# Optimization experiments

Measured on AMD Instinct MI355X. Metric: run time of the kernel, lower is better.

Reference implementation:

```python
import jax, jax.numpy as jnp
import numpy as np

N = 50000      # nodes
E = 800000     # edges
F = 64         # in_channels == out_channels
ED = 16        # edge_dim
G = 64         # graphs in batch
L = 2          # numLayers
BN_EPS = 1e-5
STD_EPS = 1e-5
AGG_DIM = F * 4 * 3  # 4 aggregators x 3 scalers


def setup_inputs() -> dict:
    key = jax.random.key(0)
    ks = jax.random.split(key, 12)
    r = lambda k, shp, fan: (jax.random.normal(k, shp, jnp.float32) / np.sqrt(fan)).astype(jnp.float32)
    return dict(
        x=jax.random.normal(ks[0], (N, F), jnp.float32),
        edge_attr=jax.random.normal(ks[1], (E, ED), jnp.float32),
        We=r(ks[2], (L, ED, F), ED), be=jnp.zeros((L, F), jnp.float32),
        Wpre=r(ks[3], (L, 3 * F, F), 3 * F), bpre=jnp.zeros((L, F), jnp.float32),
        Wpost=r(ks[4], (L, F + AGG_DIM, F), F + AGG_DIM), bpost=jnp.zeros((L, F), jnp.float32),
        Wlin=r(ks[5], (L, F, F), F), blin=jnp.zeros((L, F), jnp.float32),
        gamma=jnp.ones((L, F), jnp.float32), beta=jnp.zeros((L, F), jnp.float32),
        W1=r(ks[6], (F, 40), F), b1=jnp.zeros((40,), jnp.float32),
        W2=r(ks[7], (40, 1), 40), b2=jnp.zeros((1,), jnp.float32),
        edge_index=jax.random.randint(ks[8], (2, E), 0, N),
        batch=jnp.sort(jax.random.randint(ks[9], (N,), 0, G)),
    )


def _ceal_conv(x, src, dst, edge_attr, We, be, Wpre, bpre, Wpost, bpost, Wlin, blin, deg, amp, att):
    # PNA-style conv, towers=1, pre_layers=post_layers=1
    e = edge_attr @ We + be                                              # [E,F]
    h = jnp.concatenate([x[dst], x[src], e], axis=-1) @ Wpre + bpre      # [E,F]
    degc = jnp.maximum(deg, 1.0)[:, None]
    mean = jax.ops.segment_sum(h, dst, num_segments=N) / degc
    sq = jax.ops.segment_sum(h * h, dst, num_segments=N) / degc
    std = jnp.sqrt(jax.nn.relu(sq - mean * mean) + STD_EPS)
    has = (deg > 0)[:, None]
    mn = jnp.where(has, jax.ops.segment_min(h, dst, num_segments=N), 0.0)
    mx = jnp.where(has, jax.ops.segment_max(h, dst, num_segments=N), 0.0)
    aggs = jnp.concatenate([mean, mn, mx, std], axis=-1)                 # [N,4F]
    scaled = jnp.concatenate([aggs, aggs * amp[:, None], aggs * att[:, None]], axis=-1)  # [N,12F]
    out = jnp.concatenate([x, scaled], axis=-1) @ Wpost + bpost          # [N,F]
    return out @ Wlin + blin


def _bn(x, gamma, beta):
    mu = x.mean(0)
    var = x.var(0)  # biased, as torch BatchNorm training-mode normalization
    return (x - mu) * jax.lax.rsqrt(var + BN_EPS) * gamma + beta


def reference(x, edge_attr, We, be, Wpre, bpre, Wpost, bpost, Wlin, blin,
              gamma, beta, W1, b1, W2, b2, edge_index, batch):
    src, dst = edge_index[0], edge_index[1]
    deg = jax.ops.segment_sum(jnp.ones((E,), jnp.float32), dst, num_segments=N)
    avg_log = jnp.mean(jnp.log(deg + 1.0))
    logd = jnp.log(jnp.maximum(deg, 1.0) + 1.0)
    amp = logd / avg_log
    att = avg_log / logd
    for l in range(L):
        x = _ceal_conv(x, src, dst, edge_attr, We[l], be[l], Wpre[l], bpre[l],
                       Wpost[l], bpost[l], Wlin[l], blin[l], deg, amp, att)
        x = jax.nn.relu(_bn(x, gamma[l], beta[l]))
    cnt = jnp.maximum(jax.ops.segment_sum(jnp.ones((N,), jnp.float32), batch, num_segments=G), 1.0)
    gm = jax.ops.segment_sum(x, batch, num_segments=G) / cnt[:, None]    # global_mean_pool [G,F]
    return jax.nn.relu(gm @ W1 + b1) @ W2 + b2                           # [G,1]
```

## Files before the change

### kernel.cpp

```cpp
#include <hip/hip_runtime.h>
#include <math.h>
#include <float.h>

#define NN 50000
#define EE 800000
#define FF 64
#define EDIM 16
#define GG 64
#define NB64 782
#define NSB 196

typedef short bf16x8 __attribute__((ext_vector_type(8)));
typedef float f32x4 __attribute__((ext_vector_type(4)));

__device__ inline unsigned short bf_rne(float v) {
  unsigned int u = __float_as_uint(v);
  unsigned int r = (u + 0x7FFFu + ((u >> 16) & 1u)) >> 16;
  return (unsigned short)r;
}
__device__ inline float bf_up(unsigned short h) {
  return __uint_as_float(((unsigned int)h) << 16);
}
__device__ inline void split4(float4 v, ushort4& h, ushort4& l) {
  h.x = bf_rne(v.x); h.y = bf_rne(v.y); h.z = bf_rne(v.z); h.w = bf_rne(v.w);
  l.x = bf_rne(v.x - bf_up(h.x));
  l.y = bf_rne(v.y - bf_up(h.y));
  l.z = bf_rne(v.z - bf_up(h.z));
  l.w = bf_rne(v.w - bf_up(h.w));
}
__device__ inline float blo(unsigned int u) { return __uint_as_float(u << 16); }
__device__ inline float bhi(unsigned int u) { return __uint_as_float(u & 0xFFFF0000u); }

__global__ void k_deg(const int* __restrict__ eidx, int* __restrict__ deg) {
  int e = blockIdx.x * 256 + threadIdx.x;
  if (e < EE) atomicAdd(&deg[eidx[EE + e]], 1);
}

__global__ __launch_bounds__(256) void k_scanA(const int* __restrict__ deg, int* __restrict__ offsets,
                                               int* __restrict__ bsum, float* __restrict__ lsum) {
  __shared__ int ws[4];
  __shared__ float lw[4];
  int t = threadIdx.x;
  int lane = t & 63;
  int wv = t >> 6;
  int i = blockIdx.x * 256 + t;
  int v = (i < NN) ? deg[i] : 0;
  float lg = (i < NN) ? logf((float)v + 1.0f) : 0.0f;
  int x = v;
  #pragma unroll
  for (int o = 1; o < 64; o <<= 1) {
    int y = __shfl_up(x, o);
    if (lane >= o) x += y;
  }
  #pragma unroll
  for (int o = 1; o < 64; o <<= 1) lg += __shfl_xor(lg, o);
  if (lane == 63) ws[wv] = x;
  if (lane == 0) lw[wv] = lg;
  __syncthreads();
  int pre = 0;
  for (int k = 0; k < wv; k++) pre += ws[k];
  if (i < NN) offsets[i] = pre + x - v;
  if (t == 0) {
    bsum[blockIdx.x] = ws[0] + ws[1] + ws[2] + ws[3];
    lsum[blockIdx.x] = lw[0] + lw[1] + lw[2] + lw[3];
  }
}

__global__ __launch_bounds__(256) void k_scanB(const int* __restrict__ bsum, const float* __restrict__ lsum,
                                               int* __restrict__ bpref, float* __restrict__ meta,
                                               float* __restrict__ scbA) {
  __shared__ int ws[4];
  __shared__ float lw[4];
  int t = threadIdx.x;
  int lane = t & 63;
  int wv = t >> 6;
  int v = (t < NSB) ? bsum[t] : 0;
  float lg = (t < NSB) ? lsum[t] : 0.0f;
  int x = v;
  #pragma unroll
  for (int o = 1; o < 64; o <<= 1) {
    int y = __shfl_up(x, o);
    if (lane >= o) x += y;
  }
  #pragma unroll
  for (int o = 1; o < 64; o <<= 1) lg += __shfl_xor(lg, o);
  if (lane == 63) ws[wv] = x;
  if (lane == 0) lw[wv] = lg;
  __syncthreads();
  int pre = 0;
  for (int k = 0; k < wv; k++) pre += ws[k];
  if (t < NSB) bpref[t] = pre + x - v;
  if (t == 0) meta[0] = (lw[0] + lw[1] + lw[2] + lw[3]) / (float)NN;
  if (t < 64) { scbA[t] = 1.0f; scbA[64 + t] = 0.0f; }
  if (t == 0) scbA[128] = -FLT_MAX;
}

__global__ __launch_bounds__(256) void k_scanC(int* __restrict__ offsets, const int* __restrict__ bpref,
                                               const int* __restrict__ deg, const float* __restrict__ meta,
                                               float* __restrict__ amp, float* __restrict__ att) {
  int i = blockIdx.x * 256 + threadIdx.x;
  if (i < NN) {
    offsets[i] += bpref[blockIdx.x];
    float d = (float)deg[i];
    float avg = meta[0];
    float logd = logf(fmaxf(d, 1.0f) + 1.0f);
    amp[i] = logd / avg;
    att[i] = avg / logd;
  }
  if (i == 0) offsets[NN] = EE;
}

__global__ void k_scatter(const int* __restrict__ eidx, const int* __restrict__ offsets,
                          int* __restrict__ cursor, int* __restrict__ srcs,
                          const float* __restrict__ eattr, unsigned int* __restrict__ PermEA) {
  int e = blockIdx.x * 256 + threadIdx.x;
  if (e < EE) {
    int s = eidx[e];
    int d = eidx[EE + e];
    int pos = offsets[d] + atomicAdd(&cursor[d], 1);
    srcs[pos] = s;
    const float4* ep = (const float4*)(eattr + (size_t)e * EDIM);
    float4 q0 = ep[0], q1 = ep[1], q2 = ep[2], q3 = ep[3];
    uint4 pa, pb;
    pa.x = (unsigned)bf_rne(q0.x) | ((unsigned)bf_rne(q0.y) << 16);
    pa.y = (unsigned)bf_rne(q0.z) | ((unsigned)bf_rne(q0.w) << 16);
    pa.z = (unsigned)bf_rne(q1.x) | ((unsigned)bf_rne(q1.y) << 16);
    pa.w = (unsigned)bf_rne(q1.z) | ((unsigned)bf_rne(q1.w) << 16);
    pb.x = (unsigned)bf_rne(q2.x) | ((unsigned)bf_rne(q2.y) << 16);
    pb.y = (unsigned)bf_rne(q2.z) | ((unsigned)bf_rne(q2.w) << 16);
    pb.z = (unsigned)bf_rne(q3.x) | ((unsigned)bf_rne(q3.y) << 16);
    pb.w = (unsigned)bf_rne(q3.z) | ((unsigned)bf_rne(q3.w) << 16);
    ((uint4*)PermEA)[(size_t)pos * 2] = pa;
    ((uint4*)PermEA)[(size_t)pos * 2 + 1] = pb;
  }
}

__global__ __launch_bounds__(256) void k_prep2(const float* __restrict__ We, const float* __restrict__ be,
                                               const float* __restrict__ Wpre, const float* __restrict__ bpre,
                                               const float* __restrict__ Wpost, const float* __restrict__ bpost,
                                               const float* __restrict__ Wlin, const float* __restrict__ blin,
                                               float* __restrict__ Mw, float* __restrict__ bconst,
                                               unsigned short* __restrict__ WcT_h, unsigned short* __restrict__ WcT_l,
                                               unsigned short* __restrict__ WxT_h, unsigned short* __restrict__ WxT_l,
                                               float* __restrict__ bcomb) {
  int id = blockIdx.x * 256 + threadIdx.x;
  if (id < 53248) {
    int k = id >> 6, f = id & 63;
    float a = 0.0f;
    for (int j = 0; j < FF; j++) a += Wpost[(size_t)k * FF + j] * Wlin[j * FF + f];
    unsigned short h = bf_rne(a);
    WcT_h[f * 832 + k] = h;
    WcT_l[f * 832 + k] = bf_rne(a - bf_up(h));
  } else if (id < 61440) {
    int lid = id - 53248;
    int j = lid >> 6, k = lid & 63;
    float v = (j < 64) ? Wpre[k * FF + j] : Wpre[(64 + k) * FF + (j - 64)];
    unsigned short h = bf_rne(v);
    WxT_h[j * 64 + k] = h;
    WxT_l[j * 64 + k] = bf_rne(v - bf_up(h));
  } else if (id < 62464) {
    int lid = id - 61440;
    int k = lid >> 6, f = lid & 63;
    float a = 0.0f;
    for (int j = 0; j < FF; j++) a += We[k * FF + j] * Wpre[(128 + j) * FF + f];
    Mw[k * FF + f] = a;
  } else {
    int f = threadIdx.x;
    if (blockIdx.x == 244 && f < 64) {
      float b = bpre[f];
      for (int j = 0; j < FF; j++) b += be[j] * Wpre[(128 + j) * FF + f];
      bconst[f] = b;
      float c = blin[f];
      for (int j = 0; j < FF; j++) c += bpost[j] * Wlin[j * FF + f];
      bcomb[f] = c;
    }
  }
}

__global__ __launch_bounds__(256) void k_xform(const float* __restrict__ x, const float* __restrict__ scb,
                                               const unsigned short* __restrict__ WxT_h,
                                               const unsigned short* __restrict__ WxT_l,
                                               float* __restrict__ Xd, unsigned short* __restrict__ Xs) {
  __shared__ unsigned short Ah[64 * 72], Al[64 * 72];
  __shared__ unsigned short Bh[128 * 72], Bl[128 * 72];
  int t = threadIdx.x;
  int n0 = blockIdx.x * 64;
  {
    int j = t >> 1, half = t & 1;
    const ushort4* srch = (const ushort4*)(WxT_h + j * 64 + half * 32);
    const ushort4* srcl = (const ushort4*)(WxT_l + j * 64 + half * 32);
    #pragma unroll
    for (int i = 0; i < 8; i++) {
      *(ushort4*)&Bh[j * 72 + half * 32 + i * 4] = srch[i];
      *(ushort4*)&Bl[j * 72 + half * 32 + i * 4] = srcl[i];
    }
  }
  {
    int r = t >> 2, c0 = (t & 3) * 16;
    int n = n0 + r;
    bool rok = n < NN;
    const float4* src = (const float4*)(x + (size_t)n * FF + c0);
    float flr = scb[128];
    #pragma unroll
    for (int c4 = 0; c4 < 4; c4++) {
      float4 v = rok ? src[c4] : make_float4(0.f, 0.f, 0.f, 0.f);
      float4 sc = ((const float4*)scb)[(c0 >> 2) + c4];
      float4 of = ((const float4*)(scb + 64))[(c0 >> 2) + c4];
      v.x = fmaxf(v.x * sc.x + of.x, flr);
      v.y = fmaxf(v.y * sc.y + of.y, flr);
      v.z = fmaxf(v.z * sc.z + of.z, flr);
      v.w = fmaxf(v.w * sc.w + of.w, flr);
      ushort4 h4, l4;
      split4(v, h4, l4);
      *(ushort4*)&Ah[r * 72 + c0 + c4 * 4] = h4;
      *(ushort4*)&Al[r * 72 + c0 + c4 * 4] = l4;
    }
  }
  __syncthreads();
  int lane = t & 63;
  int l15 = lane & 15;
  int quad = lane >> 4;
  int w = __builtin_amdgcn_readfirstlane(t >> 6);
  int rbase = (w & 1) * 32;
  int cbase = (w >> 1) * 64;
  f32x4 acc[2][4];
  #pragma unroll
  for (int rt = 0; rt < 2; rt++)
    #pragma unroll
    for (int ct = 0; ct < 4; ct++) acc[rt][ct] = (f32x4){0.f, 0.f, 0.f, 0.f};

  #pragma unroll
  for (int ks = 0; ks < 2; ks++) {
    bf16x8 a_h[2], a_l[2];
    #pragma unroll
    for (int rt = 0; rt < 2; rt++) {
      int row = rbase + rt * 16 + l15;
      a_h[rt] = *(const bf16x8*)&Ah[row * 72 + ks * 32 + quad * 8];
      a_l[rt] = *(const bf16x8*)&Al[row * 72 + ks * 32 + quad * 8];
    }
    #pragma unroll
    for (int ct = 0; ct < 4; ct++) {
      int col = cbase + ct * 16 + l15;
      bf16x8 b_h = *(const bf16x8*)&Bh[col * 72 + ks * 32 + quad * 8];
      bf16x8 b_l = *(const bf16x8*)&Bl[col * 72 + ks * 32 + quad * 8];
      #pragma unroll
      for (int rt = 0; rt < 2; rt++) {
        acc[rt][ct] = __builtin_amdgcn_mfma_f32_16x16x32_bf16(a_h[rt], b_h, acc[rt][ct], 0, 0, 0);
        acc[rt][ct] = __builtin_amdgcn_mfma_f32_16x16x32_bf16(a_h[rt], b_l, acc[rt][ct], 0, 0, 0);
        acc[rt][ct] = __builtin_amdgcn_mfma_f32_16x16x32_bf16(a_l[rt], b_h, acc[rt][ct], 0, 0, 0);
      }
    }
  }
  #pragma unroll
  for (int rt = 0; rt < 2; rt++) {
    #pragma unroll
    for (int ct = 0; ct < 4; ct++) {
      int col = cbase + ct * 16 + l15;
      #pragma unroll
      for (int reg = 0; reg < 4; reg++) {
        int n = n0 + rbase + rt * 16 + quad * 4 + reg;
        if (n < NN) {
          float v = acc[rt][ct][reg];
          if (col < 64) Xd[(size_t)n * FF + col] = v;
          else          Xs[(size_t)n * FF + (col - 64)] = bf_rne(v);
        }
      }
    }
  }
}

__global__ __launch_bounds__(256) void k_agg(const int* __restrict__ srcs, const int* __restrict__ offsets,
                                             const unsigned int* __restrict__ PermEA,
                                             const float* __restrict__ Mw, const float* __restrict__ bconst,
                                             const float* __restrict__ Xd, const unsigned short* __restrict__ Xs,
                                             unsigned short* __restrict__ aggs) {
  int wid = __builtin_amdgcn_readfirstlane(threadIdx.x >> 6);
  int lane = threadIdx.x & 63;
  int n = blockIdx.x * 4 + wid;
  if (n >= NN) return;
  float mw[16];
  #pragma unroll
  for (int k = 0; k < 16; k++) mw[k] = Mw[k * FF + lane];
  float base_h = Xd[(size_t)n * FF + lane] + bconst[lane];
  int o0 = offsets[n], o1 = offsets[n + 1];
  float s = 0.f, sq = 0.f, mn = FLT_MAX, mx = -FLT_MAX;

  for (int base = o0; base < o1; base += 64) {
    int m = min(64, o1 - base);
    int sv = 0;
    if (base + lane < o1) sv = srcs[base + lane];
    for (int j = 0; j < m; j++) {
      int src = __shfl(sv, j);
      float xs = bf_up(Xs[(size_t)src * FF + lane]);
      const uint4* q = (const uint4*)PermEA + (size_t)(base + j) * 2;
      uint4 qa = q[0], qb = q[1];
      float et = blo(qa.x) * mw[0]  + bhi(qa.x) * mw[1]
               + blo(qa.y) * mw[2]  + bhi(qa.y) * mw[3]
               + blo(qa.z) * mw[4]  + bhi(qa.z) * mw[5]
               + blo(qa.w) * mw[6]  + bhi(qa.w) * mw[7]
               + blo(qb.x) * mw[8]  + bhi(qb.x) * mw[9]
               + blo(qb.y) * mw[10] + bhi(qb.y) * mw[11]
               + blo(qb.z) * mw[12] + bhi(qb.z) * mw[13]
               + blo(qb.w) * mw[14] + bhi(qb.w) * mw[15];
      float h = base_h + xs + et;
      s += h;
      sq += h * h;
      mn = fminf(mn, h);
      mx = fmaxf(mx, h);
    }
  }
  float d = (float)(o1 - o0);
  float dc = fmaxf(d, 1.0f);
  float mean = s / dc;
  float msq = sq / dc;
  float sd = sqrtf(fmaxf(msq - mean * mean, 0.0f) + 1e-5f);
  bool has = d > 0.0f;
  float vmn = has ? mn : 0.0f;
  float vmx = has ? mx : 0.0f;
  size_t b = (size_t)n * 256;
  aggs[b + lane] = bf_rne(mean);
  aggs[b + 64 + lane] = bf_rne(vmn);
  aggs[b + 128 + lane] = bf_rne(vmx);
  aggs[b + 192 + lane] = bf_rne(sd);
}

__global__ __launch_bounds__(256) void k_post(const float* __restrict__ x, const float* __restrict__ scb,
                                              const unsigned short* __restrict__ aggs,
                                              const float* __restrict__ amp, const float* __restrict__ att,
                                              const unsigned short* __restrict__ WcT_h,
                                              const unsigned short* __restrict__ WcT_l,
                                              const float* __restrict__ bcomb,
                                              float* __restrict__ y, float* __restrict__ partials) {
  __shared__ unsigned short Ah[64 * 72], Al[64 * 72];
  __shared__ unsigned short Bh[64 * 72], Bl[64 * 72];
  __shared__ float red_s[4][32], red_q[4][32];
  int t = threadIdx.x;
  int n0 = blockIdx.x * 64;
  int lane = t & 63;
  int l15 = lane & 15;
  int quad = lane >> 4;
  int w = __builtin_amdgcn_readfirstlane(t >> 6);
  int rbase = (w & 1) * 32;
  int cbase = (w >> 1) * 32;

  int ar = t >> 2;
  int ac0 = (t & 3) * 16;
  int an = n0 + ar;
  bool rok = an < NN;
  float sc_amp = rok ? amp[an] : 0.f;
  float sc_att = rok ? att[an] : 0.f;
  const float* xrow = x + (size_t)an * FF;
  const unsigned short* arow = aggs + (size_t)an * 256;
  float flr = scb[128];

  f32x4 acc[2][2];
  #pragma unroll
  for (int rt = 0; rt < 2; rt++)
    #pragma unroll
    for (int ct = 0; ct < 2; ct++) acc[rt][ct] = (f32x4){0.f, 0.f, 0.f, 0.f};

  for (int kc = 0; kc < 13; kc++) {
    if (kc == 0) {
      #pragma unroll
      for (int c4 = 0; c4 < 4; c4++) {
        float4 v = rok ? *(const float4*)(xrow + ac0 + c4 * 4) : make_float4(0.f, 0.f, 0.f, 0.f);
        float4 sc = ((const float4*)scb)[(ac0 >> 2) + c4];
        float4 of = ((const float4*)(scb + 64))[(ac0 >> 2) + c4];
        v.x = fmaxf(v.x * sc.x + of.x, flr);
        v.y = fmaxf(v.y * sc.y + of.y, flr);
        v.z = fmaxf(v.z * sc.z + of.z, flr);
        v.w = fmaxf(v.w * sc.w + of.w, flr);
        ushort4 h4, l4;
        split4(v, h4, l4);
        *(ushort4*)&Ah[ar * 72 + ac0 + c4 * 4] = h4;
        *(ushort4*)&Al[ar * 72 + ac0 + c4 * 4] = l4;
      }
    } else {
      int kcm = kc - 1;
      const unsigned short* srcb = arow + (kcm & 3) * 64;
      int sel = kcm >> 2;
      float scale = (sel == 0) ? 1.0f : (sel == 1 ? sc_amp : sc_att);
      #pragma unroll
      for (int c4 = 0; c4 < 4; c4++) {
        ushort4 u = rok ? *(const ushort4*)(srcb + ac0 + c4 * 4) : make_ushort4(0, 0, 0, 0);
        ushort4 h4;
        h4.x = bf_rne(bf_up(u.x) * scale);
        h4.y = bf_rne(bf_up(u.y) * scale);
        h4.z = bf_rne(bf_up(u.z) * scale);
        h4.w = bf_rne(bf_up(u.w) * scale);
        *(ushort4*)&Ah[ar * 72 + ac0 + c4 * 4] = h4;
      }
    }
    {
      int kbase = kc * 64;
      const ushort4* sh = (const ushort4*)(WcT_h + ar * 832 + kbase + ac0);
      const ushort4* sl = (const ushort4*)(WcT_l + ar * 832 + kbase + ac0);
      #pragma unroll
      for (int i = 0; i < 4; i++) {
        *(ushort4*)&Bh[ar * 72 + ac0 + i * 4] = sh[i];
        *(ushort4*)&Bl[ar * 72 + ac0 + i * 4] = sl[i];
      }
    }
    __syncthreads();
    bool full = (kc == 0);
    #pragma unroll
    for (int ks = 0; ks < 2; ks++) {
      bf16x8 a_h[2], a_l[2], b_h[2], b_l[2];
      #pragma unroll
      for (int rt = 0; rt < 2; rt++) {
        int row = rbase + rt * 16 + l15;
        a_h[rt] = *(const bf16x8*)&Ah[row * 72 + ks * 32 + quad * 8];
        if (full) a_l[rt] = *(const bf16x8*)&Al[row * 72 + ks * 32 + quad * 8];
      }
      #pragma unroll
      for (int ct = 0; ct < 2; ct++) {
        int col = cbase + ct * 16 + l15;
        b_h[ct] = *(const bf16x8*)&Bh[col * 72 + ks * 32 + quad * 8];
        b_l[ct] = *(const bf16x8*)&Bl[col * 72 + ks * 32 + quad * 8];
      }
      #pragma unroll
      for (int rt = 0; rt < 2; rt++)
        #pragma unroll
        for (int ct = 0; ct < 2; ct++) {
          acc[rt][ct] = __builtin_amdgcn_mfma_f32_16x16x32_bf16(a_h[rt], b_h[ct], acc[rt][ct], 0, 0, 0);
          acc[rt][ct] = __builtin_amdgcn_mfma_f32_16x16x32_bf16(a_h[rt], b_l[ct], acc[rt][ct], 0, 0, 0);
          if (full)
            acc[rt][ct] = __builtin_amdgcn_mfma_f32_16x16x32_bf16(a_l[rt], b_h[ct], acc[rt][ct], 0, 0, 0);
        }
    }
    __syncthreads();
  }

  float ps[2] = {0.f, 0.f}, pq[2] = {0.f, 0.f};
  #pragma unroll
  for (int ct = 0; ct < 2; ct++) {
    int col = cbase + ct * 16 + l15;
    float bc = bcomb[col];
    #pragma unroll
    for (int rt = 0; rt < 2; rt++) {
      #pragma unroll
      for (int reg = 0; reg < 4; reg++) {
        int n = n0 + rbase + rt * 16 + quad * 4 + reg;
        float v = acc[rt][ct][reg] + bc;
        if (n < NN) {
          y[(size_t)n * FF + col] = v;
          ps[ct] += v;
          pq[ct] += v * v;
        }
      }
    }
  }
  #pragma unroll
  for (int ct = 0; ct < 2; ct++) {
    ps[ct] += __shfl_xor(ps[ct], 16);
    ps[ct] += __shfl_xor(ps[ct], 32);
    pq[ct] += __shfl_xor(pq[ct], 16);
    pq[ct] += __shfl_xor(pq[ct], 32);
  }
  if (quad == 0) {
    #pragma unroll
    for (int ct = 0; ct < 2; ct++) {
      red_s[w][ct * 16 + l15] = ps[ct];
      red_q[w][ct * 16 + l15] = pq[ct];
    }
  }
  __syncthreads();
  if (t < 64) {
    float ss, qq;
    if (t < 32) { ss = red_s[0][t] + red_s[1][t]; qq = red_q[0][t] + red_q[1][t]; }
    else        { ss = red_s[2][t - 32] + red_s[3][t - 32]; qq = red_q[2][t - 32] + red_q[3][t - 32]; }
    partials[(size_t)blockIdx.x * 128 + t] = ss;
    partials[(size_t)blockIdx.x * 128 + 64 + t] = qq;
  }
}

__global__ __launch_bounds__(1024) void k_bnfin(const float* __restrict__ partials,
                                                const float* __restrict__ gamma, const float* __restrict__ beta,
                                                float* __restrict__ scb) {
  __shared__ float red[1024];
  __shared__ double tot[128];
  int t = threadIdx.x;
  int c = t & 127, seg = t >> 7;
  float s = 0.f;
  for (int i = seg; i < NB64; i += 8) s += partials[(size_t)i * 128 + c];
  red[t] = s;
  __syncthreads();
  if (t < 128) {
    double d = 0.0;
    #pragma unroll
    for (int sg = 0; sg < 8; sg++) d += (double)red[sg * 128 + t];
    tot[t] = d;
  }
  __syncthreads();
  if (t < 64) {
    double mu = tot[t] / (double)NN;
    double var = tot[64 + t] / (double)NN - mu * mu;
    float sc = gamma[t] * rsqrtf((float)fmax(var, 0.0) + 1e-5f);
    scb[t] = sc;
    scb[64 + t] = beta[t] - (float)mu * sc;
  }
  if (t == 0) scb[128] = 0.0f;
}

__global__ __launch_bounds__(256) void k_pool(const float* __restrict__ x, const float* __restrict__ scb,
                                              const int* __restrict__ batch,
                                              float* __restrict__ psum, float* __restrict__ cnt) {
  int lane = threadIdx.x & 63;
  int wv = threadIdx.x >> 6;
  int wglobal = blockIdx.x * 4 + wv;
  int nw = gridDim.x * 4;
  int per = (NN + nw - 1) / nw;
  int n0 = wglobal * per;
  int n1 = min(n0 + per, NN);
  if (n0 >= n1) return;
  float sc = scb[lane], of = scb[64 + lane], flr = scb[128];
  int gcur = batch[n0];
  float acc = 0.0f;
  int count = 0;
  for (int n = n0; n < n1; n++) {
    int g = batch[n];
    float v = fmaxf(x[(size_t)n * FF + lane] * sc + of, flr);
    if (g != gcur) {
      atomicAdd(&psum[gcur * FF + lane], acc);
      if (lane == 0) atomicAdd(&cnt[gcur], (float)count);
      gcur = g; acc = 0.0f; count = 0;
    }
    acc += v;
    count++;
  }
  atomicAdd(&psum[gcur * FF + lane], acc);
  if (lane == 0) atomicAdd(&cnt[gcur], (float)count);
}

__global__ void k_final(const float* __restrict__ psum, const float* __restrict__ cnt,
                        const float* __restrict__ W1, const float* __restrict__ b1,
                        const float* __restrict__ W2, const float* __restrict__ b2, float* __restrict__ out) {
  int g = threadIdx.x;
  if (g >= GG) return;
  float c = fmaxf(cnt[g], 1.0f);
  float gm[64];
  #pragma unroll
  for (int i = 0; i < 64; i++) gm[i] = psum[g * FF + i] / c;
  float o = b2[0];
  for (int h = 0; h < 40; h++) {
    float a = b1[h];
    #pragma unroll
    for (int i = 0; i < 64; i++) a += gm[i] * W1[i * 40 + h];
    o += fmaxf(a, 0.0f) * W2[h];
  }
  out[g] = o;
}

extern "C" void kernel_launch(void* const* d_in, const int* in_sizes, int n_in,
                              void* d_out, int out_size, void* d_ws, size_t ws_size,
                              hipStream_t stream) {
  (void)in_sizes; (void)n_in; (void)out_size; (void)ws_size;
  const float* x0    = (const float*)d_in[0];
  const float* eattr = (const float*)d_in[1];
  const float* We    = (const float*)d_in[2];
  const float* be    = (const float*)d_in[3];
  const float* Wpre  = (const float*)d_in[4];
  const float* bpre  = (const float*)d_in[5];
  const float* Wpost = (const float*)d_in[6];
  const float* bpost = (const float*)d_in[7];
  const float* Wlin  = (const float*)d_in[8];
  const float* blin  = (const float*)d_in[9];
  const float* gamma = (const float*)d_in[10];
  const float* beta  = (const float*)d_in[11];
  const float* W1    = (const float*)d_in[12];
  const float* b1    = (const float*)d_in[13];
  const float* W2    = (const float*)d_in[14];
  const float* b2    = (const float*)d_in[15];
  const int* eidx    = (const int*)d_in[16];
  const int* batch   = (const int*)d_in[17];
  float* out = (float*)d_out;

  char* w = (char*)d_ws;
  size_t off = 0;
  auto alloc = [&](size_t bytes) -> void* {
    void* p = w + off;
    off += bytes;
    off = (off + 255) & ~(size_t)255;
    return p;
  };
  int*    deg     = (int*)alloc(NN * sizeof(int));
  int*    offsets = (int*)alloc((NN + 1) * sizeof(int));
  int*    cursor  = (int*)alloc(NN * sizeof(int));
  int*    srcs    = (int*)alloc(EE * sizeof(int));
  unsigned int* PermEA = (unsigned int*)alloc((size_t)EE * 8 * sizeof(unsigned int));
  int*    bsum    = (int*)alloc(NSB * sizeof(int));
  int*    bpref   = (int*)alloc(NSB * sizeof(int));
  float*  lsum    = (float*)alloc(NSB * sizeof(float));
  float*  meta    = (float*)alloc(sizeof(float));
  float*  amp     = (float*)alloc(NN * sizeof(float));
  float*  att     = (float*)alloc(NN * sizeof(float));
  float*  Mw      = (float*)alloc(EDIM * FF * sizeof(float));
  float*  bconst  = (float*)alloc(FF * sizeof(float));
  float*  bcomb   = (float*)alloc(FF * sizeof(float));
  float*  scbA    = (float*)alloc(129 * sizeof(float));
  float*  scbB    = (float*)alloc(2 * 129 * sizeof(float));
  unsigned short* WcT_h = (unsigned short*)alloc(FF * 832 * sizeof(unsigned short));
  unsigned short* WcT_l = (unsigned short*)alloc(FF * 832 * sizeof(unsigned short));
  unsigned short* WxT_h = (unsigned short*)alloc(128 * 64 * sizeof(unsigned short));
  unsigned short* WxT_l = (unsigned short*)alloc(128 * 64 * sizeof(unsigned short));
  float*  partials = (float*)alloc((size_t)NB64 * 128 * sizeof(float));
  float*  Xd      = (float*)alloc((size_t)NN * FF * sizeof(float));
  unsigned short* Xs = (unsigned short*)alloc((size_t)NN * FF * sizeof(unsigned short));
  unsigned short* aggs = (unsigned short*)alloc((size_t)NN * 256 * sizeof(unsigned short));
  float*  ybuf    = (float*)alloc((size_t)NN * FF * sizeof(float));
  float*  psum    = (float*)alloc((GG * FF + GG) * sizeof(float));
  float*  cnt     = psum + GG * FF;

  hipMemsetAsync(deg, 0, NN * sizeof(int), stream);
  hipMemsetAsync(cursor, 0, NN * sizeof(int), stream);
  hipMemsetAsync(psum, 0, (GG * FF + GG) * sizeof(float), stream);

  k_deg<<<(EE + 255) / 256, 256, 0, stream>>>(eidx, deg);
  k_scanA<<<NSB, 256, 0, stream>>>(deg, offsets, bsum, lsum);
  k_scanB<<<1, 256, 0, stream>>>(bsum, lsum, bpref, meta, scbA);
  k_scanC<<<NSB, 256, 0, stream>>>(offsets, bpref, deg, meta, amp, att);
  k_scatter<<<(EE + 255) / 256, 256, 0, stream>>>(eidx, offsets, cursor, srcs, eattr, PermEA);

  const float* xin = x0;
  const float* scb_in = scbA;
  for (int l = 0; l < 2; l++) {
    k_prep2<<<245, 256, 0, stream>>>(We + l * EDIM * FF, be + l * FF, Wpre + (size_t)l * 3 * FF * FF,
                                     bpre + l * FF, Wpost + (size_t)l * 832 * FF, bpost + l * FF,
                                     Wlin + l * FF * FF, blin + l * FF,
                                     Mw, bconst, WcT_h, WcT_l, WxT_h, WxT_l, bcomb);
    k_xform<<<NB64, 256, 0, stream>>>(xin, scb_in, WxT_h, WxT_l, Xd, Xs);
    k_agg<<<(NN + 3) / 4, 256, 0, stream>>>(srcs, offsets, PermEA, Mw, bconst, Xd, Xs, aggs);
    k_post<<<NB64, 256, 0, stream>>>(xin, scb_in, aggs, amp, att, WcT_h, WcT_l, bcomb, ybuf, partials);
    k_bnfin<<<1, 1024, 0, stream>>>(partials, gamma + l * FF, beta + l * FF, scbB + l * 129);
    xin = ybuf;
    scb_in = scbB + l * 129;
  }
  k_pool<<<200, 256, 0, stream>>>(ybuf, scbB + 129, batch, psum, cnt);
  k_final<<<1, 64, 0, stream>>>(psum, cnt, W1, b1, W2, b2, out);
}
```

Before: 571.2 us.

## Compute per-edge attribute projection in k_agg with bf16 MFMA via LDS

Replaces the per-edge scalar 16-term dot product (edge attr times Mw) in the aggregation kernel with bf16 MFMA tiles over chunks of 32 edges, using a hi/lo split of Mw for extra precision. Results go to a per-wave LDS buffer that the per-edge accumulation loop then reads. The intent is to cut the VALU work and redundant PermEA loads that every lane did for every edge. In exchange it adds 32KB of LDS per block, which may limit occupancy, and wastes MFMA work on nodes with few edges. The edge-attribute buffer is padded so that tail reads stay in bounds.

New measurement: 654.3 us. 1.15x slower.

```diff
diff --git a/kernel.cpp b/kernel.cpp
--- a/kernel.cpp
+++ b/kernel.cpp
@@ -139,7 +139,8 @@
                                                const float* __restrict__ Wpre, const float* __restrict__ bpre,
                                                const float* __restrict__ Wpost, const float* __restrict__ bpost,
                                                const float* __restrict__ Wlin, const float* __restrict__ blin,
-                                               float* __restrict__ Mw, float* __restrict__ bconst,
+                                               unsigned short* __restrict__ MwT_h, unsigned short* __restrict__ MwT_l,
+                                               float* __restrict__ bconst,
                                                unsigned short* __restrict__ WcT_h, unsigned short* __restrict__ WcT_l,
                                                unsigned short* __restrict__ WxT_h, unsigned short* __restrict__ WxT_l,
                                                float* __restrict__ bcomb) {
@@ -163,7 +164,9 @@
     int k = lid >> 6, f = lid & 63;
     float a = 0.0f;
     for (int j = 0; j < FF; j++) a += We[k * FF + j] * Wpre[(128 + j) * FF + f];
-    Mw[k * FF + f] = a;
+    unsigned short h = bf_rne(a);
+    MwT_h[f * 16 + k] = h;
+    MwT_l[f * 16 + k] = bf_rne(a - bf_up(h));
   } else {
     int f = threadIdx.x;
     if (blockIdx.x == 244 && f < 64) {
@@ -271,38 +274,65 @@
 
 __global__ __launch_bounds__(256) void k_agg(const int* __restrict__ srcs, const int* __restrict__ offsets,
                                              const unsigned int* __restrict__ PermEA,
-                                             const float* __restrict__ Mw, const float* __restrict__ bconst,
+                                             const unsigned short* __restrict__ MwT_h,
+                                             const unsigned short* __restrict__ MwT_l,
+                                             const float* __restrict__ bconst,
                                              const float* __restrict__ Xd, const unsigned short* __restrict__ Xs,
                                              unsigned short* __restrict__ aggs) {
+  __shared__ float et_lds[4][32 * 64];
   int wid = __builtin_amdgcn_readfirstlane(threadIdx.x >> 6);
   int lane = threadIdx.x & 63;
+  int l15 = lane & 15;
+  int quad = lane >> 4;
   int n = blockIdx.x * 4 + wid;
   if (n >= NN) return;
-  float mw[16];
-  #pragma unroll
-  for (int k = 0; k < 16; k++) mw[k] = Mw[k * FF + lane];
+  float* et_w = et_lds[wid];
+
+  bf16x8 bh[4], bl[4];
+  #pragma unroll
+  for (int ct = 0; ct < 4; ct++) {
+    if (quad < 2) {
+      bh[ct] = *(const bf16x8*)&MwT_h[(ct * 16 + l15) * 16 + quad * 8];
+      bl[ct] = *(const bf16x8*)&MwT_l[(ct * 16 + l15) * 16 + quad * 8];
+    } else {
+      bh[ct] = (bf16x8){0, 0, 0, 0, 0, 0, 0, 0};
+      bl[ct] = (bf16x8){0, 0, 0, 0, 0, 0, 0, 0};
+    }
+  }
+
   float base_h = Xd[(size_t)n * FF + lane] + bconst[lane];
   int o0 = offsets[n], o1 = offsets[n + 1];
   float s = 0.f, sq = 0.f, mn = FLT_MAX, mx = -FLT_MAX;
 
-  for (int base = o0; base < o1; base += 64) {
-    int m = min(64, o1 - base);
-    int sv = 0;
-    if (base + lane < o1) sv = srcs[base + lane];
+  for (int base = o0; base < o1; base += 32) {
+    int m = min(32, o1 - base);
+    int idx = base + (lane & 31);
+    int sv = (idx < o1) ? srcs[idx] : 0;
+
+    #pragma unroll
+    for (int c = 0; c < 2; c++) {
+      if (c * 16 < m) {
+        int pos = base + c * 16 + l15;
+        pos = min(pos, EE - 1);
+        bf16x8 af = (bf16x8){0, 0, 0, 0, 0, 0, 0, 0};
+        if (quad < 2) af = *(const bf16x8*)(PermEA + (size_t)pos * 8 + quad * 4);
+        #pragma unroll
+        for (int ct = 0; ct < 4; ct++) {
+          f32x4 acc = (f32x4){0.f, 0.f, 0.f, 0.f};
+          acc = __builtin_amdgcn_mfma_f32_16x16x32_bf16(af, bl[ct], acc, 0, 0, 0);
+          acc = __builtin_amdgcn_mfma_f32_16x16x32_bf16(af, bh[ct], acc, 0, 0, 0);
+          int row = c * 16 + quad * 4;
+          #pragma unroll
+          for (int reg = 0; reg < 4; reg++)
+            et_w[(row + reg) * 64 + ct * 16 + l15] = acc[reg];
+        }
+      }
+    }
+
     for (int j = 0; j < m; j++) {
       int src = __shfl(sv, j);
       float xs = bf_up(Xs[(size_t)src * FF + lane]);
-      const uint4* q = (const uint4*)PermEA + (size_t)(base + j) * 2;
-      uint4 qa = q[0], qb = q[1];
-      float et = blo(qa.x) * mw[0]  + bhi(qa.x) * mw[1]
-               + blo(qa.y) * mw[2]  + bhi(qa.y) * mw[3]
-               + blo(qa.z) * mw[4]  + bhi(qa.z) * mw[5]
-               + blo(qa.w) * mw[6]  + bhi(qa.w) * mw[7]
-               + blo(qb.x) * mw[8]  + bhi(qb.x) * mw[9]
-               + blo(qb.y) * mw[10] + bhi(qb.y) * mw[11]
-               + blo(qb.z) * mw[12] + bhi(qb.z) * mw[13]
-               + blo(qb.w) * mw[14] + bhi(qb.w) * mw[15];
-      float h = base_h + xs + et;
+      float h = base_h + xs + et_w[j * 64 + lane];
       s += h;
       sq += h * h;
       mn = fminf(mn, h);
@@ -587,14 +617,15 @@
   int*    offsets = (int*)alloc((NN + 1) * sizeof(int));
   int*    cursor  = (int*)alloc(NN * sizeof(int));
   int*    srcs    = (int*)alloc(EE * sizeof(int));
-  unsigned int* PermEA = (unsigned int*)alloc((size_t)EE * 8 * sizeof(unsigned int));
+  unsigned int* PermEA = (unsigned int*)alloc(((size_t)EE + 16) * 8 * sizeof(unsigned int));
   int*    bsum    = (int*)alloc(NSB * sizeof(int));
   int*    bpref   = (int*)alloc(NSB * sizeof(int));
   float*  lsum    = (float*)alloc(NSB * sizeof(float));
   float*  meta    = (float*)alloc(sizeof(float));
   float*  amp     = (float*)alloc(NN * sizeof(float));
   float*  att     = (float*)alloc(NN * sizeof(float));
-  float*  Mw      = (float*)alloc(EDIM * FF * sizeof(float));
+  unsigned short* MwT_h = (unsigned short*)alloc(FF * EDIM * sizeof(unsigned short));
+  unsigned short* MwT_l = (unsigned short*)alloc(FF * EDIM * sizeof(unsigned short));
   float*  bconst  = (float*)alloc(FF * sizeof(float));
   float*  bcomb   = (float*)alloc(FF * sizeof(float));
   float*  scbA    = (float*)alloc(129 * sizeof(float));
@@ -627,9 +658,9 @@
     k_prep2<<<245, 256, 0, stream>>>(We + l * EDIM * FF, be + l * FF, Wpre + (size_t)l * 3 * FF * FF,
                                      bpre + l * FF, Wpost + (size_t)l * 832 * FF, bpost + l * FF,
                                      Wlin + l * FF * FF, blin + l * FF,
-                                     Mw, bconst, WcT_h, WcT_l, WxT_h, WxT_l, bcomb);
+                                     MwT_h, MwT_l, bconst, WcT_h, WcT_l, WxT_h, WxT_l, bcomb);
     k_xform<<<NB64, 256, 0, stream>>>(xin, scb_in, WxT_h, WxT_l, Xd, Xs);
-    k_agg<<<(NN + 3) / 4, 256, 0, stream>>>(srcs, offsets, PermEA, Mw, bconst, Xd, Xs, aggs);
+    k_agg<<<(NN + 3) / 4, 256, 0, stream>>>(srcs, offsets, PermEA, MwT_h, MwT_l, bconst, Xd, Xs, aggs);
     k_post<<<NB64, 256, 0, stream>>>(xin, scb_in, aggs, amp, att, WcT_h, WcT_l, bcomb, ybuf, partials);
     k_bnfin<<<1, 1024, 0, stream>>>(partials, gamma + l * FF, beta + l * FF, scbB + l * 129);
     xin = ybuf;
```
